# Performance work log

Hardware: AMD Instinct MI355X
Metric: run time of the kernel (lower is better)

## Reference

```python
import jax, jax.numpy as jnp
import numpy as np

SLOPE = 0.01   # LeakyReLU default negative slope
EPS = 1e-5     # InstanceNorm eps
PAD = 6        # shift-search border

def _pad(x):
    # ReplicationPad (1,1) on H and W (depth pad is 0, depth==1 anyway)
    return jnp.pad(x, ((0, 0), (0, 0), (1, 1), (1, 1)), mode='edge')

def _conv(x, w, b):
    y = jax.lax.conv_general_dilated(x, w, (1, 1), 'VALID',
                                     dimension_numbers=('NCHW', 'OIHW', 'NCHW'))
    return y + b[None, :, None, None]

def _inorm(x):
    # InstanceNorm3d (affine=False) over (D,H,W); D==1 so over (H,W) per (b,c)
    m = jnp.mean(x, axis=(-2, -1), keepdims=True)
    v = jnp.mean((x - m) ** 2, axis=(-2, -1), keepdims=True)
    return (x - m) * jax.lax.rsqrt(v + EPS)

def _lrelu(x):
    return jnp.where(x >= 0, x, SLOPE * x)

def setup_inputs() -> dict:
    key = jax.random.key(0)
    ks = jax.random.split(key, 8)
    B, H, W = 8, 256, 256
    xIn = jax.random.normal(ks[0], (B, 1, H, W), jnp.float32)
    target = jax.random.normal(ks[1], (B, 1, H, W), jnp.float32)
    w0 = jax.random.normal(ks[2], (64, 1, 3, 3), jnp.float32) * 0.1
    b0 = jax.random.normal(ks[3], (64,), jnp.float32) * 0.1
    ws = jax.random.normal(ks[4], (7, 64, 64, 3, 3), jnp.float32) * 0.05
    bs = jax.random.normal(ks[5], (7, 64), jnp.float32) * 0.05
    wp = jax.random.normal(ks[6], (1, 64, 3, 3), jnp.float32) * 0.05
    bp = jax.random.normal(ks[7], (1,), jnp.float32) * 0.05
    return {'xIn': xIn, 'target': target, 'w0': w0, 'b0': b0,
            'ws': ws, 'bs': bs, 'wp': wp, 'bp': bp}

def reference(xIn, target, w0, b0, ws, bs, wp, bp):
    x = _lrelu(_inorm(_conv(_pad(xIn), w0, b0)))
    for i in range(7):
        x = _lrelu(_inorm(_conv(_pad(x), ws[i], bs[i])))
    # projection + residual
    hr = _conv(_pad(x), wp, bp) + xIn  # (B,1,H,W)

    # vectorized findBestLoss: 13x13 shift search
    B, C, H, W = hr.shape
    h, w = H - 2 * PAD, W - 2 * PAD
    t = hr.dtype.type(0) + target[..., PAD:H - PAD, PAD:W - PAD]  # (B,C,h,w)
    offs = jnp.stack(jnp.meshgrid(jnp.arange(13), jnp.arange(13),
                                  indexing='ij'), -1).reshape(-1, 2)  # (169,2)

    def _slice(off):
        return jax.lax.dynamic_slice(hr, (0, 0, off[0], off[1]), (B, C, h, w))

    crops = jax.vmap(_slice)(offs)  # (169,B,C,h,w)
    eq = jax.lax.stop_gradient(
        jnp.mean(t[None] - crops, axis=(2, 3, 4), keepdims=True))  # detached equalizer
    losses = jnp.mean((crops + eq - t[None]) ** 2, axis=(2, 3, 4))  # (169,B)
    loss = jnp.mean(jnp.min(losses, axis=0))
    return hr, loss
```

## Files before the change

kernel.cpp:

```cpp
#include <hip/hip_runtime.h>

#define B_ 8
#define C_ 64
#define HW_ 65536
#define SLOPE_ 0.01f
#define EPS_ 1e-5f
#define CROP_ 244
#define NPIX_ 59536.0f

typedef unsigned short u16;
typedef __attribute__((ext_vector_type(8))) _Float16 f16x8;
typedef __attribute__((ext_vector_type(2))) _Float16 f16x2;
typedef __attribute__((ext_vector_type(4))) float f32x4;

__device__ __forceinline__ int clampi(int v, int lo, int hi) { return v < lo ? lo : (v > hi ? hi : v); }

__device__ __forceinline__ u16 f2h(float f) {
    union { _Float16 h; u16 u; } v; v.h = (_Float16)f; return v.u;
}
__device__ __forceinline__ float h2f(u16 b) {
    union { u16 u; _Float16 h; } v; v.u = b; return (float)v.h;
}
__device__ __forceinline__ f16x2 lrelu2(f16x2 a) {
    const f16x2 z = {(_Float16)0.f, (_Float16)0.f};
    const f16x2 sl = {(_Float16)SLOPE_, (_Float16)SLOPE_};
    return __builtin_elementwise_max(a, z) + sl * __builtin_elementwise_min(a, z);
}

__global__ void wtrans_kernel(const float* __restrict__ ws, u16* __restrict__ wH) {
    int idx = blockIdx.x * 256 + threadIdx.x;
    if (idx >= 7 * 36864) return;
    int l = idx / 36864;
    int rem = idx - l * 36864;
    int frag = rem >> 9;
    int lj = rem & 511;
    int lane = lj >> 3, j = lj & 7;
    int tap = frag >> 3, kb = (frag >> 2) & 1, mt = frag & 3;
    int oc = (mt << 4) + (lane & 15);
    int ic = (kb << 5) + ((lane >> 4) << 3) + j;
    wH[idx] = f2h(ws[((l * 64 + oc) * 64 + ic) * 9 + tap]);
}

__global__ __launch_bounds__(256) void conv0_kernel(
    const float* __restrict__ xin, const float* __restrict__ w0,
    const float* __restrict__ b0, u16* __restrict__ yout) {
    __shared__ float w0s[576];
    __shared__ float b0s[64];
    int tid = threadIdx.x;
    for (int i = tid; i < 576; i += 256) w0s[i] = w0[i];
    if (tid < 64) b0s[tid] = b0[tid];
    __syncthreads();
    int b = blockIdx.x & 7;
    int px = (blockIdx.x >> 3) * 256 + tid;
    int pxg = (b << 16) + px;
    int y = px >> 8, x = px & 255;
    float xv[9];
#pragma unroll
    for (int ky = 0; ky < 3; ky++)
#pragma unroll
        for (int kx = 0; kx < 3; kx++)
            xv[ky * 3 + kx] = xin[(b << 16) + (clampi(y + ky - 1, 0, 255) << 8) + clampi(x + kx - 1, 0, 255)];
    float acc[64];
#pragma unroll
    for (int k = 0; k < 64; k++) acc[k] = b0s[k];
#pragma unroll
    for (int t = 0; t < 9; t++) {
        float v = xv[t];
#pragma unroll
        for (int k = 0; k < 64; k++) acc[k] = fmaf(v, w0s[k * 9 + t], acc[k]);
    }
    uint4* op = (uint4*)(yout + ((size_t)pxg << 6));
#pragma unroll
    for (int c8 = 0; c8 < 8; c8++) {
        uint4 o;
        o.x = (unsigned)f2h(acc[c8 * 8 + 0]) | ((unsigned)f2h(acc[c8 * 8 + 1]) << 16);
        o.y = (unsigned)f2h(acc[c8 * 8 + 2]) | ((unsigned)f2h(acc[c8 * 8 + 3]) << 16);
        o.z = (unsigned)f2h(acc[c8 * 8 + 4]) | ((unsigned)f2h(acc[c8 * 8 + 5]) << 16);
        o.w = (unsigned)f2h(acc[c8 * 8 + 6]) | ((unsigned)f2h(acc[c8 * 8 + 7]) << 16);
        op[c8] = o;
    }
}

__global__ __launch_bounds__(256) void stats0_kernel(const u16* __restrict__ yin, float* __restrict__ partial) {
    __shared__ float red[4][64][2];
    int tid = threadIdx.x;
    int b = blockIdx.x & 7, tile = blockIdx.x >> 3;
    int pxl = tid >> 3, c8 = tid & 7;
    float s[8], s2[8];
#pragma unroll
    for (int i = 0; i < 8; i++) { s[i] = 0.f; s2[i] = 0.f; }
    for (int it = 0; it < 8; it++) {
        int px = (tile << 8) + (it << 5) + pxl;
        f16x8 v = *(const f16x8*)(yin + ((((size_t)(b << 16)) + px) << 6) + (c8 << 3));
#pragma unroll
        for (int i = 0; i < 8; i++) {
            float f = (float)v[i];
            s[i] += f; s2[i] += f * f;
        }
    }
#pragma unroll
    for (int msk = 8; msk <= 32; msk <<= 1)
#pragma unroll
        for (int i = 0; i < 8; i++) {
            s[i] += __shfl_xor(s[i], msk);
            s2[i] += __shfl_xor(s2[i], msk);
        }
    int lane = tid & 63, wv = tid >> 6;
    if (lane < 8) {
#pragma unroll
        for (int i = 0; i < 8; i++) {
            red[wv][lane * 8 + i][0] = s[i];
            red[wv][lane * 8 + i][1] = s2[i];
        }
    }
    __syncthreads();
    if (tid < 128) {
        int oc = tid >> 1, k2 = tid & 1;
        float v = red[0][oc][k2] + red[1][oc][k2] + red[2][oc][k2] + red[3][oc][k2];
        partial[(((b << 8) + tile) << 7) + (oc << 1) + k2] = v;
    }
}

__global__ __launch_bounds__(64) void statfin_kernel(const float* __restrict__ partial, float* __restrict__ normp, int ntiles) {
    int b = blockIdx.x >> 6, oc = blockIdx.x & 63;
    int lane = threadIdx.x;
    float s = 0.f, s2 = 0.f;
    for (int t = lane; t < ntiles; t += 64) {
        const float* p = partial + (((size_t)(b * ntiles + t)) << 7) + (oc << 1);
        s += p[0]; s2 += p[1];
    }
#pragma unroll
    for (int msk = 1; msk < 64; msk <<= 1) { s += __shfl_xor(s, msk); s2 += __shfl_xor(s2, msk); }
    if (lane == 0) {
        float mean = s * (1.0f / HW_);
        float var = s2 * (1.0f / HW_) - mean * mean;
        float inv = rsqrtf(var + EPS_);
        normp[blockIdx.x * 2] = inv;
        normp[blockIdx.x * 2 + 1] = -mean * inv;
    }
}

__global__ __launch_bounds__(256, 2) void conv_mid_kernel(
    const u16* __restrict__ yin, const float* __restrict__ normp,
    const u16* __restrict__ wH, const float* __restrict__ bias,
    u16* __restrict__ yout, float* __restrict__ partial) {
    __shared__ u16 s_in[612 * 64];
    __shared__ unsigned s_invk[32];
    __shared__ unsigned s_betak[32];
    __shared__ float s_bias[64];
    float* s_red = (float*)s_in;

    int tid = threadIdx.x;
    int b = blockIdx.x & 7;
    int tile = blockIdx.x >> 3;
    int ty = tile >> 4, tx = tile & 15;
    int y0 = ty << 5, x0 = tx << 4;

    if (tid < 64) s_bias[tid] = bias[tid];
    if (tid < 32) {
        float4 ld = ((const float4*)(normp + (b << 7)))[tid];
        union { unsigned u; f16x2 h; } iv, bv;
        iv.h = (f16x2){(_Float16)ld.x, (_Float16)ld.z};
        bv.h = (f16x2){(_Float16)ld.y, (_Float16)ld.w};
        s_invk[tid] = iv.u;
        s_betak[tid] = bv.u;
    }
    __syncthreads();

    for (int chunk = tid; chunk < 4896; chunk += 256) {
        int px = chunk >> 3, c8 = chunk & 7;
        int row = px / 18;
        int col = px - row * 18;
        int iy = clampi(y0 - 1 + row, 0, 255);
        int ix = clampi(x0 - 1 + col, 0, 255);
        union { uint4 q; f16x2 h2[4]; } ui, uo;
        ui.q = *(const uint4*)(yin + ((((size_t)(b << 16)) + (iy << 8) + ix) << 6) + (c8 << 3));
#pragma unroll
        for (int p = 0; p < 4; p++) {
            union { unsigned u; f16x2 h; } iv, bv;
            iv.u = s_invk[(c8 << 2) + p];
            bv.u = s_betak[(c8 << 2) + p];
            uo.h2[p] = lrelu2(ui.h2[p] * iv.h + bv.h);
        }
        int phys = c8 ^ (px & 7);
        *(uint4*)(&s_in[(px << 6) + (phys << 3)]) = uo.q;
    }
    __syncthreads();

    int lane = tid & 63, wv = tid >> 6;
    int m = lane & 15, q = lane >> 4;
    int r0 = wv << 3;

    f32x4 acc[4][8];
#pragma unroll
    for (int a = 0; a < 4; a++)
#pragma unroll
        for (int c = 0; c < 8; c++) acc[a][c] = (f32x4){0.f, 0.f, 0.f, 0.f};

    const f16x8* wfp = (const f16x8*)wH;
#pragma unroll 1
    for (int t = 0; t < 9; t++) {
        int ky = t / 3, kx = t - ky * 3;
        const f16x8* wn = wfp + (t << 9);
        f16x8 wf[8];
#pragma unroll
        for (int f = 0; f < 8; f++) wf[f] = wn[(f << 6) + lane];
#pragma unroll
        for (int nt = 0; nt < 8; nt++) {
            int p = (r0 + nt + ky) * 18 + kx + m;
            int key = p & 7;
            const u16* pin = &s_in[p << 6];
            f16x8 bf0 = *(const f16x8*)(pin + ((q ^ key) << 3));
            f16x8 bf1 = *(const f16x8*)(pin + (((4 + q) ^ key) << 3));
#pragma unroll
            for (int mt = 0; mt < 4; mt++)
                acc[mt][nt] = __builtin_amdgcn_mfma_f32_16x16x32_f16(wf[mt], bf0, acc[mt][nt], 0, 0, 0);
#pragma unroll
            for (int mt = 0; mt < 4; mt++)
                acc[mt][nt] = __builtin_amdgcn_mfma_f32_16x16x32_f16(wf[4 + mt], bf1, acc[mt][nt], 0, 0, 0);
        }
    }
    __syncthreads();

    float ss[4][4], sq[4][4];
#pragma unroll
    for (int mt = 0; mt < 4; mt++)
#pragma unroll
        for (int r = 0; r < 4; r++) { ss[mt][r] = 0.f; sq[mt][r] = 0.f; }

#pragma unroll
    for (int mt = 0; mt < 4; mt++) {
        int ocb = (mt << 4) + (q << 2);
        float b0v = s_bias[ocb], b1v = s_bias[ocb + 1], b2v = s_bias[ocb + 2], b3v = s_bias[ocb + 3];
#pragma unroll
        for (int nt = 0; nt < 8; nt++) {
            f32x4 v = acc[mt][nt];
            float v0 = v.x + b0v, v1 = v.y + b1v, v2 = v.z + b2v, v3 = v.w + b3v;
            uint2 o;
            o.x = (unsigned)f2h(v0) | ((unsigned)f2h(v1) << 16);
            o.y = (unsigned)f2h(v2) | ((unsigned)f2h(v3) << 16);
            int y = y0 + r0 + nt, x = x0 + m;
            *(uint2*)(yout + ((((size_t)(b << 16)) + (y << 8) + x) << 6) + ocb) = o;
            ss[mt][0] += v0; ss[mt][1] += v1; ss[mt][2] += v2; ss[mt][3] += v3;
            sq[mt][0] += v0 * v0; sq[mt][1] += v1 * v1; sq[mt][2] += v2 * v2; sq[mt][3] += v3 * v3;
        }
    }
#pragma unroll
    for (int mt = 0; mt < 4; mt++)
#pragma unroll
        for (int r = 0; r < 4; r++) {
#pragma unroll
            for (int msk = 1; msk <= 8; msk <<= 1) {
                ss[mt][r] += __shfl_xor(ss[mt][r], msk);
                sq[mt][r] += __shfl_xor(sq[mt][r], msk);
            }
        }
    if (m == 0) {
#pragma unroll
        for (int mt = 0; mt < 4; mt++)
#pragma unroll
            for (int r = 0; r < 4; r++) {
                int oc = (mt << 4) + (q << 2) + r;
                s_red[(wv * 64 + oc) * 2] = ss[mt][r];
                s_red[(wv * 64 + oc) * 2 + 1] = sq[mt][r];
            }
    }
    __syncthreads();
    if (tid < 128) {
        int oc = tid >> 1, k2 = tid & 1;
        float v = s_red[(0 * 64 + oc) * 2 + k2] + s_red[(1 * 64 + oc) * 2 + k2]
                + s_red[(2 * 64 + oc) * 2 + k2] + s_red[(3 * 64 + oc) * 2 + k2];
        partial[(((b << 7) + tile) << 7) + (oc << 1) + k2] = v;
    }
}

__global__ __launch_bounds__(256) void proj_kernel(
    const u16* __restrict__ y7, const float* __restrict__ normp,
    const float* __restrict__ wp, const float* __restrict__ bp,
    const float* __restrict__ xin, float* __restrict__ out) {
    __shared__ u16 s_a[18 * 66 * 8];
    __shared__ unsigned s_invk[32];
    __shared__ unsigned s_betak[32];
    __shared__ unsigned s_w2[288];

    int tid = threadIdx.x;
    int b = blockIdx.x & 7, slab = blockIdx.x >> 3;
    int sy = slab >> 2, sx = slab & 3;
    int y0 = sy << 4, x0 = sx << 6;

    if (tid < 32) {
        float4 ld = ((const float4*)(normp + (b << 7)))[tid];
        union { unsigned u; f16x2 h; } iv, bv;
        iv.h = (f16x2){(_Float16)ld.x, (_Float16)ld.z};
        bv.h = (f16x2){(_Float16)ld.y, (_Float16)ld.w};
        s_invk[tid] = iv.u;
        s_betak[tid] = bv.u;
    }
    for (int i = tid; i < 288; i += 256) {
        int pr = i / 9, tap = i - pr * 9;
        int ch = pr << 1;
        s_w2[i] = (unsigned)f2h(wp[ch * 9 + tap]) | ((unsigned)f2h(wp[(ch + 1) * 9 + tap]) << 16);
    }
    __syncthreads();

    int col = tid & 63, prow = tid >> 6;
    float acc[4];
#pragma unroll
    for (int r = 0; r < 4; r++) acc[r] = bp[0];

    for (int c8 = 0; c8 < 8; c8++) {
        for (int idx = tid; idx < 1188; idx += 256) {
            int row = idx / 66;
            int cc = idx - row * 66;
            int iy = clampi(y0 - 1 + row, 0, 255);
            int ix = clampi(x0 - 1 + cc, 0, 255);
            union { uint4 q; f16x2 h2[4]; } ui, uo;
            ui.q = *(const uint4*)(y7 + ((((size_t)(b << 16)) + (iy << 8) + ix) << 6) + (c8 << 3));
#pragma unroll
            for (int p = 0; p < 4; p++) {
                union { unsigned u; f16x2 h; } iv, bv;
                iv.u = s_invk[(c8 << 2) + p];
                bv.u = s_betak[(c8 << 2) + p];
                uo.h2[p] = lrelu2(ui.h2[p] * iv.h + bv.h);
            }
            *(uint4*)(&s_a[idx << 3]) = uo.q;
        }
        __syncthreads();

#pragma unroll
        for (int ky = 0; ky < 3; ky++)
#pragma unroll
            for (int kx = 0; kx < 3; kx++) {
                int tap = ky * 3 + kx;
                float w[8];
#pragma unroll
                for (int p = 0; p < 4; p++) {
                    unsigned wu = s_w2[((c8 << 2) + p) * 9 + tap];
                    w[2 * p] = h2f((u16)(wu & 0xffff));
                    w[2 * p + 1] = h2f((u16)(wu >> 16));
                }
#pragma unroll
                for (int rr = 0; rr < 4; rr++) {
                    int lrow = prow * 4 + rr + ky;
                    f16x8 v = *(const f16x8*)(&s_a[(lrow * 66 + col + kx) << 3]);
#pragma unroll
                    for (int i = 0; i < 8; i++)
                        acc[rr] = fmaf((float)v[i], w[i], acc[rr]);
                }
            }
        __syncthreads();
    }

#pragma unroll
    for (int rr = 0; rr < 4; rr++) {
        int pxg = (b << 16) + ((y0 + prow * 4 + rr) << 8) + x0 + col;
        out[pxg] = acc[rr] + xin[pxg];
    }
}

__global__ __launch_bounds__(256) void loss_strip_kernel(
    const float* __restrict__ hr, const float* __restrict__ target,
    float* __restrict__ partial2) {
    __shared__ float s_hr[4][256];
    __shared__ float s_t[4][244];
    __shared__ float s_r2[4][13][2];

    int tid = threadIdx.x;
    int b = blockIdx.x & 7;
    int rest = blockIdx.x >> 3;
    int oy = rest % 13;
    int strip = rest / 13;
    int y0 = strip << 2;

    for (int i = tid; i < 1024; i += 256) {
        int r = i >> 8, x = i & 255;
        s_hr[r][x] = hr[(b << 16) + ((y0 + oy + r) << 8) + x];
    }
    for (int i = tid; i < 976; i += 256) {
        int r = i / 244, x = i - r * 244;
        s_t[r][x] = target[(b << 16) + ((y0 + r + 6) << 8) + 6 + x];
    }
    __syncthreads();

    float s[13], s2[13];
#pragma unroll
    for (int o = 0; o < 13; o++) { s[o] = 0.f; s2[o] = 0.f; }
    if (tid < 244) {
#pragma unroll
        for (int r = 0; r < 4; r++) {
            float tv = s_t[r][tid];
#pragma unroll
            for (int o = 0; o < 13; o++) {
                float d = s_hr[r][tid + o] - tv;
                s[o] += d; s2[o] += d * d;
            }
        }
    }
#pragma unroll
    for (int msk = 1; msk < 64; msk <<= 1)
#pragma unroll
        for (int o = 0; o < 13; o++) {
            s[o] += __shfl_xor(s[o], msk);
            s2[o] += __shfl_xor(s2[o], msk);
        }
    int lane = tid & 63, wv = tid >> 6;
    if (lane == 0) {
#pragma unroll
        for (int o = 0; o < 13; o++) { s_r2[wv][o][0] = s[o]; s_r2[wv][o][1] = s2[o]; }
    }
    __syncthreads();
    if (tid < 26) {
        int o = tid >> 1, k = tid & 1;
        float v = s_r2[0][o][k] + s_r2[1][o][k] + s_r2[2][o][k] + s_r2[3][o][k];
        int off = oy * 13 + o;
        partial2[(((b * 61 + strip) * 169) + off) * 2 + k] = v;
    }
}

__global__ __launch_bounds__(64) void loss_mid_kernel(
    const float* __restrict__ partial2, float* __restrict__ lossM) {
    int b = blockIdx.x & 7, off = blockIdx.x >> 3;
    int lane = threadIdx.x;
    float s = 0.f, s2 = 0.f;
    if (lane < 61) {
        const float* p = partial2 + (((b * 61 + lane) * 169) + off) * 2;
        s = p[0]; s2 = p[1];
    }
#pragma unroll
    for (int msk = 1; msk < 64; msk <<= 1) { s += __shfl_xor(s, msk); s2 += __shfl_xor(s2, msk); }
    if (lane == 0) {
        float m = s * (1.0f / NPIX_);
        lossM[off * 8 + b] = s2 * (1.0f / NPIX_) - m * m;
    }
}

__global__ void loss_final_kernel(const float* __restrict__ lossM, float* __restrict__ out) {
    int b = threadIdx.x;
    float mn = 0.f;
    if (b < 8) {
        mn = 1e30f;
        for (int off = 0; off < 169; off++) mn = fminf(mn, lossM[off * 8 + b]);
    }
#pragma unroll
    for (int msk = 1; msk < 8; msk <<= 1) mn += __shfl_xor(mn, msk);
    if (b == 0) out[0] = mn * 0.125f;
}

extern "C" void kernel_launch(void* const* d_in, const int* in_sizes, int n_in,
                              void* d_out, int out_size, void* d_ws, size_t ws_size,
                              hipStream_t stream) {
    const float* xIn    = (const float*)d_in[0];
    const float* target = (const float*)d_in[1];
    const float* w0     = (const float*)d_in[2];
    const float* b0     = (const float*)d_in[3];
    const float* wsAll  = (const float*)d_in[4];
    const float* bsAll  = (const float*)d_in[5];
    const float* wp     = (const float*)d_in[6];
    const float* bp     = (const float*)d_in[7];
    float* out = (float*)d_out;

    float* normp    = (float*)d_ws;
    float* partial  = normp + 1024;
    float* partial2 = partial + 262144;
    float* lossM    = partial2 + 164944;
    u16*  wH        = (u16*)(lossM + 1352);
    u16*  bufA      = wH + 258048;
    u16*  bufB      = bufA + 33554432;

    wtrans_kernel<<<1008, 256, 0, stream>>>(wsAll, wH);
    conv0_kernel<<<2048, 256, 0, stream>>>(xIn, w0, b0, bufA);
    stats0_kernel<<<2048, 256, 0, stream>>>(bufA, partial);
    statfin_kernel<<<512, 64, 0, stream>>>(partial, normp, 256);
    for (int l = 0; l < 7; l++) {
        const u16* in = (l & 1) ? bufB : bufA;
        u16* o = (l & 1) ? bufA : bufB;
        conv_mid_kernel<<<1024, 256, 0, stream>>>(
            in, normp, wH + l * 36864, bsAll + l * 64, o, partial);
        statfin_kernel<<<512, 64, 0, stream>>>(partial, normp, 128);
    }
    proj_kernel<<<512, 256, 0, stream>>>(bufB, normp, wp, bp, xIn, out);
    loss_strip_kernel<<<6344, 256, 0, stream>>>(out, target, partial2);
    loss_mid_kernel<<<1352, 64, 0, stream>>>(partial2, lossM);
    loss_final_kernel<<<1, 64, 0, stream>>>(lossM, out + 524288);
}
```

Measured before the change: 730.0 us.

## Make mid conv loop over four row tiles with LDS weights and register prefetch

The mid-layer convolution now launches a quarter as many blocks; each processes four vertically stacked tiles, keeps the full layer weights in shared memory, and prefetches the next tile's activations into registers during the MFMA work. This removes repeated global weight fetches and tries to hide input load latency. The projection kernel stages all 64 channels at once into a swizzled shared tile and computes two pixels per thread, removing its per-channel-group sync loop. The cost is far lower occupancy in the conv (one block per CU, large LDS) and higher register use.

```diff
diff --git a/kernel.cpp b/kernel.cpp
--- a/kernel.cpp
+++ b/kernel.cpp
@@ -140,21 +140,24 @@
     }
 }
 
-__global__ __launch_bounds__(256, 2) void conv_mid_kernel(
+#define CM_CHUNKS 4896
+__global__ __launch_bounds__(256, 1) void conv_mid_kernel(
     const u16* __restrict__ yin, const float* __restrict__ normp,
     const u16* __restrict__ wH, const float* __restrict__ bias,
     u16* __restrict__ yout, float* __restrict__ partial) {
+    __shared__ u16 s_w[36864];
     __shared__ u16 s_in[612 * 64];
+    __shared__ float s_red[4 * 64 * 2];
     __shared__ unsigned s_invk[32];
     __shared__ unsigned s_betak[32];
     __shared__ float s_bias[64];
-    float* s_red = (float*)s_in;
 
     int tid = threadIdx.x;
-    int b = blockIdx.x & 7;
-    int tile = blockIdx.x >> 3;
-    int ty = tile >> 4, tx = tile & 15;
-    int y0 = ty << 5, x0 = tx << 4;
+    int bid = blockIdx.x;
+    int b = bid & 7;
+    int xs = (bid >> 3) & 15;
+    int yq = bid >> 7;
+    int x0 = xs << 4;
 
     if (tid < 64) s_bias[tid] = bias[tid];
     if (tid < 32) {
@@ -165,25 +168,29 @@
         s_invk[tid] = iv.u;
         s_betak[tid] = bv.u;
     }
-    __syncthreads();
-
-    for (int chunk = tid; chunk < 4896; chunk += 256) {
-        int px = chunk >> 3, c8 = chunk & 7;
-        int row = px / 18;
-        int col = px - row * 18;
-        int iy = clampi(y0 - 1 + row, 0, 255);
-        int ix = clampi(x0 - 1 + col, 0, 255);
-        union { uint4 q; f16x2 h2[4]; } ui, uo;
-        ui.q = *(const uint4*)(yin + ((((size_t)(b << 16)) + (iy << 8) + ix) << 6) + (c8 << 3));
-#pragma unroll
-        for (int p = 0; p < 4; p++) {
-            union { unsigned u; f16x2 h; } iv, bv;
-            iv.u = s_invk[(c8 << 2) + p];
-            bv.u = s_betak[(c8 << 2) + p];
-            uo.h2[p] = lrelu2(ui.h2[p] * iv.h + bv.h);
-        }
-        int phys = c8 ^ (px & 7);
-        *(uint4*)(&s_in[(px << 6) + (phys << 3)]) = uo.q;
+    for (int i = tid; i < 4608; i += 256)
+        ((uint4*)s_w)[i] = ((const uint4*)wH)[i];
+    __syncthreads();
+
+    {
+        int y0 = yq << 7;
+        for (int chunk = tid; chunk < CM_CHUNKS; chunk += 256) {
+            int px = chunk >> 3, c8 = chunk & 7;
+            int row = px / 18;
+            int col = px - row * 18;
+            int iy = clampi(y0 - 1 + row, 0, 255);
+            int ix = clampi(x0 - 1 + col, 0, 255);
+            union { uint4 q; f16x2 h2[4]; } ui, uo;
+            ui.q = *(const uint4*)(yin + ((((size_t)(b << 16)) + (iy << 8) + ix) << 6) + (c8 << 3));
+#pragma unroll
+            for (int p = 0; p < 4; p++) {
+                union { unsigned u; f16x2 h; } iv, bv;
+                iv.u = s_invk[(c8 << 2) + p];
+                bv.u = s_betak[(c8 << 2) + p];
+                uo.h2[p] = lrelu2(ui.h2[p] * iv.h + bv.h);
+            }
+            *(uint4*)(&s_in[(px << 6) + ((c8 ^ (px & 7)) << 3)]) = uo.q;
+        }
     }
     __syncthreads();
 
@@ -191,102 +198,141 @@
     int m = lane & 15, q = lane >> 4;
     int r0 = wv << 3;
 
-    f32x4 acc[4][8];
-#pragma unroll
-    for (int a = 0; a < 4; a++)
-#pragma unroll
-        for (int c = 0; c < 8; c++) acc[a][c] = (f32x4){0.f, 0.f, 0.f, 0.f};
-
-    const f16x8* wfp = (const f16x8*)wH;
+    for (int r = 0; r < 4; r++) {
+        int y0 = ((yq << 2) + r) << 5;
+        uint4 pf[20];
+        if (r < 3) {
+            int y0n = y0 + 32;
+#pragma unroll
+            for (int k = 0; k < 20; k++) {
+                int chunk = tid + (k << 8);
+                if (chunk < CM_CHUNKS) {
+                    int px = chunk >> 3, c8 = chunk & 7;
+                    int row = px / 18;
+                    int col = px - row * 18;
+                    int iy = clampi(y0n - 1 + row, 0, 255);
+                    int ix = clampi(x0 - 1 + col, 0, 255);
+                    pf[k] = *(const uint4*)(yin + ((((size_t)(b << 16)) + (iy << 8) + ix) << 6) + (c8 << 3));
+                }
+            }
+        }
+
+        f32x4 acc[4][8];
+#pragma unroll
+        for (int a = 0; a < 4; a++)
+#pragma unroll
+            for (int c = 0; c < 8; c++) acc[a][c] = (f32x4){0.f, 0.f, 0.f, 0.f};
+
 #pragma unroll 1
-    for (int t = 0; t < 9; t++) {
-        int ky = t / 3, kx = t - ky * 3;
-        const f16x8* wn = wfp + (t << 9);
-        f16x8 wf[8];
-#pragma unroll
-        for (int f = 0; f < 8; f++) wf[f] = wn[(f << 6) + lane];
-#pragma unroll
-        for (int nt = 0; nt < 8; nt++) {
-            int p = (r0 + nt + ky) * 18 + kx + m;
-            int key = p & 7;
-            const u16* pin = &s_in[p << 6];
-            f16x8 bf0 = *(const f16x8*)(pin + ((q ^ key) << 3));
-            f16x8 bf1 = *(const f16x8*)(pin + (((4 + q) ^ key) << 3));
+        for (int t = 0; t < 9; t++) {
+            int ky = t / 3, kx = t - ky * 3;
+            f16x8 wf[8];
+#pragma unroll
+            for (int f = 0; f < 8; f++)
+                wf[f] = *(const f16x8*)(&s_w[(t << 12) + (f << 9) + (lane << 3)]);
+#pragma unroll
+            for (int nt = 0; nt < 8; nt++) {
+                int p = (r0 + nt + ky) * 18 + kx + m;
+                int key = p & 7;
+                const u16* pin = &s_in[p << 6];
+                f16x8 bf0 = *(const f16x8*)(pin + ((q ^ key) << 3));
+                f16x8 bf1 = *(const f16x8*)(pin + (((4 + q) ^ key) << 3));
+#pragma unroll
+                for (int mt = 0; mt < 4; mt++)
+                    acc[mt][nt] = __builtin_amdgcn_mfma_f32_16x16x32_f16(wf[mt], bf0, acc[mt][nt], 0, 0, 0);
+#pragma unroll
+                for (int mt = 0; mt < 4; mt++)
+                    acc[mt][nt] = __builtin_amdgcn_mfma_f32_16x16x32_f16(wf[4 + mt], bf1, acc[mt][nt], 0, 0, 0);
+            }
+        }
+
+        float ss[4][4], sq[4][4];
+#pragma unroll
+        for (int mt = 0; mt < 4; mt++)
+#pragma unroll
+            for (int rr = 0; rr < 4; rr++) { ss[mt][rr] = 0.f; sq[mt][rr] = 0.f; }
+
+#pragma unroll
+        for (int mt = 0; mt < 4; mt++) {
+            int ocb = (mt << 4) + (q << 2);
+            float b0v = s_bias[ocb], b1v = s_bias[ocb + 1], b2v = s_bias[ocb + 2], b3v = s_bias[ocb + 3];
+#pragma unroll
+            for (int nt = 0; nt < 8; nt++) {
+                f32x4 v = acc[mt][nt];
+                float v0 = v.x + b0v, v1 = v.y + b1v, v2 = v.z + b2v, v3 = v.w + b3v;
+                uint2 o;
+                o.x = (unsigned)f2h(v0) | ((unsigned)f2h(v1) << 16);
+                o.y = (unsigned)f2h(v2) | ((unsigned)f2h(v3) << 16);
+                int y = y0 + r0 + nt, x = x0 + m;
+                *(uint2*)(yout + ((((size_t)(b << 16)) + (y << 8) + x) << 6) + ocb) = o;
+                ss[mt][0] += v0; ss[mt][1] += v1; ss[mt][2] += v2; ss[mt][3] += v3;
+                sq[mt][0] += v0 * v0; sq[mt][1] += v1 * v1; sq[mt][2] += v2 * v2; sq[mt][3] += v3 * v3;
+            }
+        }
+#pragma unroll
+        for (int mt = 0; mt < 4; mt++)
+#pragma unroll
+            for (int rr = 0; rr < 4; rr++) {
+#pragma unroll
+                for (int msk = 1; msk <= 8; msk <<= 1) {
+                    ss[mt][rr] += __shfl_xor(ss[mt][rr], msk);
+                    sq[mt][rr] += __shfl_xor(sq[mt][rr], msk);
+                }
+            }
+        if (m == 0) {
 #pragma unroll
             for (int mt = 0; mt < 4; mt++)
-                acc[mt][nt] = __builtin_amdgcn_mfma_f32_16x16x32_f16(wf[mt], bf0, acc[mt][nt], 0, 0, 0);
-#pragma unroll
-            for (int mt = 0; mt < 4; mt++)
-                acc[mt][nt] = __builtin_amdgcn_mfma_f32_16x16x32_f16(wf[4 + mt], bf1, acc[mt][nt], 0, 0, 0);
-        }
-    }
-    __syncthreads();
-
-    float ss[4][4], sq[4][4];
-#pragma unroll
-    for (int mt = 0; mt < 4; mt++)
-#pragma unroll
-        for (int r = 0; r < 4; r++) { ss[mt][r] = 0.f; sq[mt][r] = 0.f; }
-
-#pragma unroll
-    for (int mt = 0; mt < 4; mt++) {
-        int ocb = (mt << 4) + (q << 2);
-        float b0v = s_bias[ocb], b1v = s_bias[ocb + 1], b2v = s_bias[ocb + 2], b3v = s_bias[ocb + 3];
-#pragma unroll
-        for (int nt = 0; nt < 8; nt++) {
-            f32x4 v = acc[mt][nt];
-            float v0 = v.x + b0v, v1 = v.y + b1v, v2 = v.z + b2v, v3 = v.w + b3v;
-            uint2 o;
-            o.x = (unsigned)f2h(v0) | ((unsigned)f2h(v1) << 16);
-            o.y = (unsigned)f2h(v2) | ((unsigned)f2h(v3) << 16);
-            int y = y0 + r0 + nt, x = x0 + m;
-            *(uint2*)(yout + ((((size_t)(b << 16)) + (y << 8) + x) << 6) + ocb) = o;
-            ss[mt][0] += v0; ss[mt][1] += v1; ss[mt][2] += v2; ss[mt][3] += v3;
-            sq[mt][0] += v0 * v0; sq[mt][1] += v1 * v1; sq[mt][2] += v2 * v2; sq[mt][3] += v3 * v3;
-        }
-    }
-#pragma unroll
-    for (int mt = 0; mt < 4; mt++)
-#pragma unroll
-        for (int r = 0; r < 4; r++) {
-#pragma unroll
-            for (int msk = 1; msk <= 8; msk <<= 1) {
-                ss[mt][r] += __shfl_xor(ss[mt][r], msk);
-                sq[mt][r] += __shfl_xor(sq[mt][r], msk);
-            }
-        }
-    if (m == 0) {
-#pragma unroll
-        for (int mt = 0; mt < 4; mt++)
-#pragma unroll
-            for (int r = 0; r < 4; r++) {
-                int oc = (mt << 4) + (q << 2) + r;
-                s_red[(wv * 64 + oc) * 2] = ss[mt][r];
-                s_red[(wv * 64 + oc) * 2 + 1] = sq[mt][r];
-            }
-    }
-    __syncthreads();
-    if (tid < 128) {
-        int oc = tid >> 1, k2 = tid & 1;
-        float v = s_red[(0 * 64 + oc) * 2 + k2] + s_red[(1 * 64 + oc) * 2 + k2]
-                + s_red[(2 * 64 + oc) * 2 + k2] + s_red[(3 * 64 + oc) * 2 + k2];
-        partial[(((b << 7) + tile) << 7) + (oc << 1) + k2] = v;
-    }
-}
-
-__global__ __launch_bounds__(256) void proj_kernel(
+#pragma unroll
+                for (int rr = 0; rr < 4; rr++) {
+                    int oc = (mt << 4) + (q << 2) + rr;
+                    s_red[(wv * 64 + oc) * 2] = ss[mt][rr];
+                    s_red[(wv * 64 + oc) * 2 + 1] = sq[mt][rr];
+                }
+        }
+        __syncthreads();
+        if (tid < 128) {
+            int oc = tid >> 1, k2 = tid & 1;
+            float v = s_red[(0 * 64 + oc) * 2 + k2] + s_red[(1 * 64 + oc) * 2 + k2]
+                    + s_red[(2 * 64 + oc) * 2 + k2] + s_red[(3 * 64 + oc) * 2 + k2];
+            int tile = (((yq << 2) + r) << 4) + xs;
+            partial[(((b << 7) + tile) << 7) + (oc << 1) + k2] = v;
+        }
+        if (r < 3) {
+#pragma unroll
+            for (int k = 0; k < 20; k++) {
+                int chunk = tid + (k << 8);
+                if (chunk < CM_CHUNKS) {
+                    int px = chunk >> 3, c8 = chunk & 7;
+                    union { uint4 q; f16x2 h2[4]; } ui, uo;
+                    ui.q = pf[k];
+#pragma unroll
+                    for (int p = 0; p < 4; p++) {
+                        union { unsigned u; f16x2 h; } iv, bv;
+                        iv.u = s_invk[(c8 << 2) + p];
+                        bv.u = s_betak[(c8 << 2) + p];
+                        uo.h2[p] = lrelu2(ui.h2[p] * iv.h + bv.h);
+                    }
+                    *(uint4*)(&s_in[(px << 6) + ((c8 ^ (px & 7)) << 3)]) = uo.q;
+                }
+            }
+        }
+        __syncthreads();
+    }
+}
+
+__global__ __launch_bounds__(256, 2) void proj_kernel(
     const u16* __restrict__ y7, const float* __restrict__ normp,
     const float* __restrict__ wp, const float* __restrict__ bp,
     const float* __restrict__ xin, float* __restrict__ out) {
-    __shared__ u16 s_a[18 * 66 * 8];
+    __shared__ u16 s_a[612 * 64];
     __shared__ unsigned s_invk[32];
     __shared__ unsigned s_betak[32];
     __shared__ unsigned s_w2[288];
 
     int tid = threadIdx.x;
-    int b = blockIdx.x & 7, slab = blockIdx.x >> 3;
-    int sy = slab >> 2, sx = slab & 3;
-    int y0 = sy << 4, x0 = sx << 6;
+    int b = blockIdx.x & 7, t = blockIdx.x >> 3;
+    int ys = t >> 3, xsp = t & 7;
+    int y0 = ys << 4, x0 = xsp << 5;
 
     if (tid < 32) {
         float4 ld = ((const float4*)(normp + (b << 7)))[tid];
@@ -303,58 +349,52 @@
     }
     __syncthreads();
 
-    int col = tid & 63, prow = tid >> 6;
-    float acc[4];
-#pragma unroll
-    for (int r = 0; r < 4; r++) acc[r] = bp[0];
-
-    for (int c8 = 0; c8 < 8; c8++) {
-        for (int idx = tid; idx < 1188; idx += 256) {
-            int row = idx / 66;
-            int cc = idx - row * 66;
-            int iy = clampi(y0 - 1 + row, 0, 255);
-            int ix = clampi(x0 - 1 + cc, 0, 255);
-            union { uint4 q; f16x2 h2[4]; } ui, uo;
-            ui.q = *(const uint4*)(y7 + ((((size_t)(b << 16)) + (iy << 8) + ix) << 6) + (c8 << 3));
-#pragma unroll
-            for (int p = 0; p < 4; p++) {
-                union { unsigned u; f16x2 h; } iv, bv;
-                iv.u = s_invk[(c8 << 2) + p];
-                bv.u = s_betak[(c8 << 2) + p];
-                uo.h2[p] = lrelu2(ui.h2[p] * iv.h + bv.h);
-            }
-            *(uint4*)(&s_a[idx << 3]) = uo.q;
-        }
-        __syncthreads();
-
+    for (int chunk = tid; chunk < 4896; chunk += 256) {
+        int px = chunk >> 3, c8 = chunk & 7;
+        int row = px / 34;
+        int col = px - row * 34;
+        int iy = clampi(y0 - 1 + row, 0, 255);
+        int ix = clampi(x0 - 1 + col, 0, 255);
+        union { uint4 q; f16x2 h2[4]; } ui, uo;
+        ui.q = *(const uint4*)(y7 + ((((size_t)(b << 16)) + (iy << 8) + ix) << 6) + (c8 << 3));
+#pragma unroll
+        for (int p = 0; p < 4; p++) {
+            union { unsigned u; f16x2 h; } iv, bv;
+            iv.u = s_invk[(c8 << 2) + p];
+            bv.u = s_betak[(c8 << 2) + p];
+            uo.h2[p] = lrelu2(ui.h2[p] * iv.h + bv.h);
+        }
+        *(uint4*)(&s_a[(px << 6) + ((c8 ^ (px & 7)) << 3)]) = uo.q;
+    }
+    __syncthreads();
+
+    float bias0 = bp[0];
+#pragma unroll
+    for (int half = 0; half < 2; half++) {
+        int idx = (half << 8) + tid;
+        int py = idx >> 5, pxx = idx & 31;
+        float acc = bias0;
 #pragma unroll
         for (int ky = 0; ky < 3; ky++)
 #pragma unroll
             for (int kx = 0; kx < 3; kx++) {
+                int p = (py + ky) * 34 + pxx + kx;
+                int key = p & 7;
+                const u16* pin = &s_a[p << 6];
                 int tap = ky * 3 + kx;
-                float w[8];
-#pragma unroll
-                for (int p = 0; p < 4; p++) {
-                    unsigned wu = s_w2[((c8 << 2) + p) * 9 + tap];
-                    w[2 * p] = h2f((u16)(wu & 0xffff));
-                    w[2 * p + 1] = h2f((u16)(wu >> 16));
+#pragma unroll
+                for (int c8 = 0; c8 < 8; c8++) {
+                    f16x8 v = *(const f16x8*)(pin + ((c8 ^ key) << 3));
+#pragma unroll
+                    for (int i2 = 0; i2 < 4; i2++) {
+                        unsigned wu = s_w2[((c8 << 2) + i2) * 9 + tap];
+                        acc = fmaf((float)v[2 * i2], h2f((u16)(wu & 0xffff)), acc);
+                        acc = fmaf((float)v[2 * i2 + 1], h2f((u16)(wu >> 16)), acc);
+                    }
                 }
-#pragma unroll
-                for (int rr = 0; rr < 4; rr++) {
-                    int lrow = prow * 4 + rr + ky;
-                    f16x8 v = *(const f16x8*)(&s_a[(lrow * 66 + col + kx) << 3]);
-#pragma unroll
-                    for (int i = 0; i < 8; i++)
-                        acc[rr] = fmaf((float)v[i], w[i], acc[rr]);
-                }
-            }
-        __syncthreads();
-    }
-
-#pragma unroll
-    for (int rr = 0; rr < 4; rr++) {
-        int pxg = (b << 16) + ((y0 + prow * 4 + rr) << 8) + x0 + col;
-        out[pxg] = acc[rr] + xin[pxg];
+            }
+        int pxg = (b << 16) + ((y0 + py) << 8) + x0 + pxx;
+        out[pxg] = acc + xin[pxg];
     }
 }
 
@@ -474,11 +514,11 @@
     for (int l = 0; l < 7; l++) {
         const u16* in = (l & 1) ? bufB : bufA;
         u16* o = (l & 1) ? bufA : bufB;
-        conv_mid_kernel<<<1024, 256, 0, stream>>>(
+        conv_mid_kernel<<<256, 256, 0, stream>>>(
             in, normp, wH + l * 36864, bsAll + l * 64, o, partial);
         statfin_kernel<<<512, 64, 0, stream>>>(partial, normp, 128);
     }
-    proj_kernel<<<512, 256, 0, stream>>>(bufB, normp, wp, bp, xIn, out);
+    proj_kernel<<<1024, 256, 0, stream>>>(bufB, normp, wp, bp, xIn, out);
     loss_strip_kernel<<<6344, 256, 0, stream>>>(out, target, partial2);
     loss_mid_kernel<<<1352, 64, 0, stream>>>(partial2, lossM);
     loss_final_kernel<<<1, 64, 0, stream>>>(lossM, out + 524288);
```

After: 795.1 us. 1.09x slower.
